# Kernel optimization log

Measured on AMD Instinct MI355X. Metric: run time of the kernel, lower is better.

Reference implementation:

```python
import jax, jax.numpy as jnp
import numpy as np

B, L, F, P = 128, 256, 4, 4   # dialogs, dialog length, future/past links
IN, H, C = 1024, 256, 7
N = B * L


def _build_edges():
    # same structure as build_intra_graph: self-loop + F future + P past per node
    i = np.arange(L)
    ss, tt = [], []
    for d in range(-P, F + 1):
        j = i + d
        m = (j >= 0) & (j < L)
        ss.append(i[m]); tt.append(j[m])
    s = np.concatenate(ss); t = np.concatenate(tt)
    offs = (np.arange(B) * L)[:, None]
    S = (s[None, :] + offs).ravel()
    T = (t[None, :] + offs).ravel()
    return np.stack([S, T]).astype(np.int32)


def setup_inputs() -> dict:
    key = jax.random.key(0)
    ks = jax.random.split(key, 16)
    ei = _build_edges()
    speakers = np.asarray(jax.random.randint(ks[0], (N,), 0, 2), dtype=np.int32)
    rel = (speakers[ei[0]] * speakers[ei[1]]).astype(np.int32)
    sd_in = 1.0 / np.sqrt(IN)
    sd_h = 1.0 / np.sqrt(H)
    return {
        "input": jax.random.normal(ks[1], (N, IN), jnp.float32),
        "dialog_lengths": jnp.full((B,), L, jnp.int32),
        "speakers": jnp.asarray(speakers),
        "labels": jax.random.randint(ks[2], (N,), 0, C, jnp.int32),
        "edge_index": jnp.asarray(ei),
        "rel_type": jnp.asarray(rel),
        # RGCNConv(IN, H, num_relations=2): per-relation weight, root weight, bias
        "W_rgcn": jax.random.normal(ks[3], (2, IN, H), jnp.float32) * sd_in,
        "W_root": jax.random.normal(ks[4], (IN, H), jnp.float32) * sd_in,
        "b_rgcn": jax.random.normal(ks[5], (H,), jnp.float32) * 0.01,
        # GraphConv(H, H): lin_rel (on aggregated neighbors, with bias), lin_root (no bias)
        "W_rel": jax.random.normal(ks[6], (H, H), jnp.float32) * sd_h,
        "b_rel": jax.random.normal(ks[7], (H,), jnp.float32) * 0.01,
        "W_grt": jax.random.normal(ks[8], (H, H), jnp.float32) * sd_h,
        # skip_con: Linear(IN, H)
        "W_skip": jax.random.normal(ks[9], (IN, H), jnp.float32) * sd_in,
        "b_skip": jax.random.normal(ks[10], (H,), jnp.float32) * 0.01,
        # classify: Linear(H, C)
        "W_cls": jax.random.normal(ks[11], (H, C), jnp.float32) * sd_h,
        "b_cls": jax.random.normal(ks[12], (C,), jnp.float32) * 0.01,
    }


def reference(input, dialog_lengths, speakers, labels, edge_index, rel_type,
              W_rgcn, W_root, b_rgcn, W_rel, b_rel, W_grt,
              W_skip, b_skip, W_cls, b_cls):
    n = input.shape[0]
    src, dst = edge_index[0], edge_index[1]
    seg = jax.ops.segment_sum

    # --- RGCNConv: out_i = x_i @ W_root + b + sum_r mean_{j in N_r(i)} x_j @ W_r
    t = jnp.einsum('ni,rio->rno', input, W_rgcn)      # [2, N, H]
    msg = t[rel_type, src]                            # [E, H] relation-specific messages
    h = input @ W_root + b_rgcn
    for r in range(2):
        m = (rel_type == r).astype(input.dtype)       # [E]
        s = seg(msg * m[:, None], dst, num_segments=n)
        cnt = seg(m, dst, num_segments=n)
        h = h + s / jnp.maximum(cnt, 1.0)[:, None]    # mean aggregation per relation

    # --- GraphConv (aggr='add'): out_i = W_rel @ sum_j h_j + b_rel + W_grt @ h_i
    neigh = seg(h[src], dst, num_segments=n)          # [N, H]
    h2 = neigh @ W_rel + b_rel + h @ W_grt

    # --- skip connection + classifier
    out = (h2 + input @ W_skip + b_skip) @ W_cls + b_cls  # [N, C]

    # --- cross entropy (mean)
    logp = jax.nn.log_softmax(out, axis=-1)
    loss = -jnp.mean(jnp.take_along_axis(logp, labels[:, None].astype(jnp.int32), axis=1))
    return out, loss
```

## Files before the change

### kernel.cpp

```cpp
#include <hip/hip_runtime.h>

#define NN 32768
#define INF 1024
#define HF 256

typedef __bf16 bf16x8 __attribute__((ext_vector_type(8)));
typedef float f32x4 __attribute__((ext_vector_type(4)));
typedef unsigned short u16x8 __attribute__((ext_vector_type(8)));

__device__ __forceinline__ float bf2f(unsigned short u) {
  union { unsigned int i; float f; } v; v.i = ((unsigned int)u) << 16; return v.f;
}
__device__ __forceinline__ unsigned short f2bf(float f) {
  union { float f; unsigned int i; } v; v.f = f;
  unsigned int x = v.i;
  return (unsigned short)((x + 0x7fffu + ((x >> 16) & 1u)) >> 16);
}

__device__ __forceinline__ void ld_lds16(const unsigned short* g, unsigned short* l) {
  __builtin_amdgcn_global_load_lds(
      (__attribute__((address_space(1))) const unsigned int*)g,
      (__attribute__((address_space(3))) unsigned int*)l, 16, 0, 0);
}
__device__ __forceinline__ void ld_lds16v(const void* g, void* l) {
  __builtin_amdgcn_global_load_lds(
      (__attribute__((address_space(1))) const unsigned int*)g,
      (__attribute__((address_space(3))) unsigned int*)l, 16, 0, 0);
}

__device__ __forceinline__ bf16x8 cvt8(f32x4 lo, f32x4 hi) {
  union { unsigned int u[4]; bf16x8 v; } r;
  asm("v_cvt_pk_bf16_f32 %0, %1, %2" : "=v"(r.u[0]) : "v"(lo[0]), "v"(lo[1]));
  asm("v_cvt_pk_bf16_f32 %0, %1, %2" : "=v"(r.u[1]) : "v"(lo[2]), "v"(lo[3]));
  asm("v_cvt_pk_bf16_f32 %0, %1, %2" : "=v"(r.u[2]) : "v"(hi[0]), "v"(hi[1]));
  asm("v_cvt_pk_bf16_f32 %0, %1, %2" : "=v"(r.u[3]) : "v"(hi[2]), "v"(hi[3]));
  return r.v;
}

__global__ __launch_bounds__(256)
void diagcn_prep(const float* __restrict__ Wrgcn, const float* __restrict__ Wroot,
                 const float* __restrict__ Wskip, const float* __restrict__ Wgrt,
                 const float* __restrict__ Wrel, unsigned short* __restrict__ WbigT,
                 unsigned short* __restrict__ WsmT, float* __restrict__ loss) {
  int tb = blockIdx.x;
  if (tb == 0 && threadIdx.x == 0) loss[0] = 0.f;
  __shared__ float tile[64 * 65];
  const float* src;
  int k0, ncol0;
  unsigned short* dst;
  int ldd, nrow0;
  if (tb < 256) {
    int tn = tb >> 4, tk = tb & 15;
    int mat = tn >> 2;
    src = (mat == 0) ? Wrgcn : (mat == 1) ? (Wrgcn + 262144) : (mat == 2) ? Wroot : Wskip;
    k0 = tk * 64; ncol0 = (tn & 3) * 64;
    dst = WbigT; ldd = 1024; nrow0 = tn * 64;
  } else {
    int t2 = tb - 256;
    int tn = t2 >> 3, tk = t2 & 7;
    src = (tk < 4) ? Wgrt : Wrel;
    k0 = (tk & 3) * 64; ncol0 = tn * 64;
    dst = WsmT; ldd = 512; nrow0 = tn * 64;
  }
  int kdst0 = (tb < 256) ? k0 : (((tb - 256) & 7) * 64);
  int c = threadIdx.x & 63, rb = threadIdx.x >> 6;
#pragma unroll
  for (int it = 0; it < 16; ++it) {
    int r = rb + it * 4;
    tile[r * 65 + c] = src[(size_t)(k0 + r) * 256 + ncol0 + c];
  }
  __syncthreads();
  int kk = threadIdx.x & 63;
#pragma unroll
  for (int it = 0; it < 16; ++it) {
    int nn = rb + it * 4;
    dst[(size_t)(nrow0 + nn) * ldd + kdst0 + kk] = f2bf(tile[kk * 65 + nn]);
  }
}

__global__ __launch_bounds__(512, 1)
void diagcn_gemm1(const float* __restrict__ X, const unsigned short* __restrict__ BT,
                  unsigned short* __restrict__ Y) {
  __shared__ unsigned short SH[73728];
  const int tid = threadIdx.x;
  const int w = tid >> 6, lane = tid & 63;
  const int quad = lane >> 4, l15 = lane & 15;
  const int wm = w >> 2, wn = w & 3;
  const int b = blockIdx.x;
  const int wg = ((b & 7) << 6) + (b >> 3);
  const int m0 = (wg >> 2) << 8;
  const int n0 = (wg & 3) << 8;
  const int bbase = wn * 64 + l15;
  const int sw8 = ((quad ^ ((l15 >> 1) & 3)) << 3);
  const int csrc8 = (((lane & 3) ^ ((lane >> 3) & 3)) << 3);
  const float* gAf = X + (size_t)(m0 + w * 32 + (lane >> 3)) * 1024
                       + (((lane & 7) ^ (lane >> 3)) << 2);
  const unsigned short* gB0 = BT + (size_t)(n0 + w * 32 + (lane >> 2)) * 1024 + csrc8;
  const int c1o = (((2 * quad) ^ (l15 & 7)) << 2);
  const int c2o = c1o ^ 4;

  f32x4 acc[8][4] = {};

#define G1_STAGE(t, buf)                                                       \
  {                                                                            \
    unsigned short* aB = SH + (buf) * 24576 + w * 2048;                        \
    const float* gs = gAf + (t) * 32;                                          \
    ld_lds16v(gs,             aB);                                             \
    ld_lds16v(gs +  8 * 1024, aB +  512);                                      \
    ld_lds16v(gs + 16 * 1024, aB + 1024);                                      \
    ld_lds16v(gs + 24 * 1024, aB + 1536);                                      \
    unsigned short* bB = SH + (buf) * 24576 + 16384 + w * 1024;                \
    const unsigned short* gb = gB0 + (t) * 32;                                 \
    ld_lds16(gb, bB);                                                          \
    ld_lds16(gb + 16 * 1024, bB + 512);                                        \
  }

#define G1_COMPUTE(buf)                                                       \
  {                                                                           \
    const float* Af = (const float*)(SH + (buf) * 24576);                     \
    const unsigned short* Bs = SH + (buf) * 24576 + 16384;                    \
    bf16x8 bv[4];                                                             \
    _Pragma("unroll")                                                         \
    for (int j = 0; j < 4; ++j)                                               \
      bv[j] = *(const bf16x8*)&Bs[(bbase + j * 16) * 32 + sw8];               \
    __builtin_amdgcn_s_setprio(1);                                            \
    _Pragma("unroll")                                                         \
    for (int i = 0; i < 8; ++i) {                                             \
      int ra = wm * 128 + i * 16 + l15;                                       \
      const float* rp = Af + ra * 32;                                         \
      f32x4 lo = *(const f32x4*)(rp + c1o);                                   \
      f32x4 hi = *(const f32x4*)(rp + c2o);                                   \
      bf16x8 av = cvt8(lo, hi);                                               \
      _Pragma("unroll")                                                       \
      for (int j = 0; j < 4; ++j)                                             \
        acc[i][j] = __builtin_amdgcn_mfma_f32_16x16x32_bf16(av, bv[j], acc[i][j], 0, 0, 0); \
    }                                                                         \
    __builtin_amdgcn_s_setprio(0);                                            \
  }

  G1_STAGE(0, 0);
  G1_STAGE(1, 1);
  asm volatile("s_waitcnt vmcnt(6)" ::: "memory");
  __builtin_amdgcn_s_barrier();

#pragma unroll 1
  for (int t = 0; t < 30; ++t) {
    G1_STAGE(t + 2, (t + 2) % 3);
    G1_COMPUTE(t % 3);
    asm volatile("s_waitcnt vmcnt(6)" ::: "memory");
    __builtin_amdgcn_s_barrier();
  }
  G1_COMPUTE(0);
  asm volatile("s_waitcnt vmcnt(0)" ::: "memory");
  __builtin_amdgcn_s_barrier();
  G1_COMPUTE(1);
#undef G1_STAGE
#undef G1_COMPUTE

#pragma unroll
  for (int i = 0; i < 8; ++i)
#pragma unroll
    for (int j = 0; j < 4; ++j) {
      const int row = m0 + wm * 128 + i * 16 + quad * 4;
      const int col = n0 + wn * 64 + j * 16 + l15;
#pragma unroll
      for (int r = 0; r < 4; ++r)
        Y[(size_t)(row + r) * 1024 + col] = f2bf(acc[i][j][r]);
    }
}

__global__ __launch_bounds__(256)
void diagcn_h(const unsigned short* __restrict__ Y, const int* __restrict__ spk,
              const float* __restrict__ brgcn, unsigned short* __restrict__ A2) {
  int b = blockIdx.x;
  int wv = threadIdx.x >> 6, lane = threadIdx.x & 63;
  int half = lane >> 5, li = lane & 31, c0 = li << 3;
  int node = ((b & 7) << 12) + ((b >> 3) << 3) + wv * 2 + half;
  int p = node & 255, dbase = node - p;
  int si = spk[node];
  float a0[8] = {}, a1[8] = {};
  float n0 = 0.f, n1 = 0.f;
#pragma unroll
  for (int d = -4; d <= 4; ++d) {
    int pj = p + d;
    float w = (pj >= 0 && pj < 256) ? 1.f : 0.f;
    int jc = pj < 0 ? 0 : (pj > 255 ? 255 : pj);
    int nj = dbase + jc;
    int rel = si & spk[nj];
    u16x8 v = *(const u16x8*)&Y[(size_t)nj * 1024 + (rel << 8) + c0];
    float w1 = rel ? w : 0.f, w0 = rel ? 0.f : w;
#pragma unroll
    for (int k = 0; k < 8; ++k) {
      float f = bf2f(v[k]);
      a0[k] += f * w0; a1[k] += f * w1;
    }
    n0 += w0; n1 += w1;
  }
  u16x8 vr = *(const u16x8*)&Y[(size_t)node * 1024 + 512 + c0];
  float i0 = 1.f / fmaxf(n0, 1.f), i1 = 1.f / fmaxf(n1, 1.f);
  u16x8 u;
#pragma unroll
  for (int k = 0; k < 8; ++k)
    u[k] = f2bf(bf2f(vr[k]) + brgcn[c0 + k] + a0[k] * i0 + a1[k] * i1);
  *(u16x8*)&A2[(size_t)node * 512 + c0] = u;
}

__global__ __launch_bounds__(256)
void diagcn_neigh(unsigned short* __restrict__ A2) {
  int b = blockIdx.x;
  int wv = threadIdx.x >> 6, lane = threadIdx.x & 63;
  int half = lane >> 5, li = lane & 31, c0 = li << 3;
  int node = ((b & 7) << 12) + ((b >> 3) << 3) + wv * 2 + half;
  int p = node & 255, dbase = node - p;
  float s[8] = {};
#pragma unroll
  for (int d = -4; d <= 4; ++d) {
    int pj = p + d;
    float w = (pj >= 0 && pj < 256) ? 1.f : 0.f;
    int jc = pj < 0 ? 0 : (pj > 255 ? 255 : pj);
    u16x8 v = *(const u16x8*)&A2[(size_t)(dbase + jc) * 512 + c0];
#pragma unroll
    for (int k = 0; k < 8; ++k) s[k] += bf2f(v[k]) * w;
  }
  u16x8 u;
#pragma unroll
  for (int k = 0; k < 8; ++k) u[k] = f2bf(s[k]);
  *(u16x8*)&A2[(size_t)node * 512 + 256 + c0] = u;
}

__global__ __launch_bounds__(256)
void diagcn_gemm2(const unsigned short* __restrict__ A, const unsigned short* __restrict__ BT,
                  const unsigned short* __restrict__ Y, const float* __restrict__ Wcls,
                  const float* __restrict__ bcls, const float* __restrict__ brel,
                  const float* __restrict__ bskip, const int* __restrict__ labels,
                  float* __restrict__ out, float* __restrict__ loss) {
  const int K = 512;
  __shared__ unsigned short SH[40960];
  const int tid = threadIdx.x;
  const int w = tid >> 6, lane = tid & 63;
  const int quad = lane >> 4, l15 = lane & 15;
  const int b = blockIdx.x;
  const int m0 = (((b & 7) << 6) + (b >> 3)) << 6;
  const int rowg = lane >> 3;
  const int kbsw = (lane & 7) ^ rowg;

  f32x4 acc[16] = {};
  const unsigned short* Abase = A + (size_t)m0 * K + kbsw * 8;
  const unsigned short* Bbase = BT + kbsw * 8;
  const unsigned short* Ybase = Y + (size_t)(m0 + (lane >> 5)) * 1024 + 768 + (lane & 31) * 8;

#define G2_STAGE(t, buf)                                                        \
  {                                                                             \
    unsigned short* As_ = SH + (buf) * 20480;                                   \
    unsigned short* Bs_ = As_ + 4096;                                           \
    int k0_ = (t) * 64;                                                         \
    _Pragma("unroll")                                                           \
    for (int i = 0; i < 2; ++i) {                                               \
      int grp = w * 2 + i;                                                      \
      ld_lds16(Abase + (size_t)(grp * 8 + rowg) * K + k0_, &As_[grp * 512]);    \
    }                                                                           \
    _Pragma("unroll")                                                           \
    for (int i = 0; i < 8; ++i) {                                               \
      int grp = w * 8 + i;                                                      \
      ld_lds16(Bbase + (size_t)(grp * 8 + rowg) * K + k0_, &Bs_[grp * 512]);    \
    }                                                                           \
  }
#define G2_COMPUTE(buf)                                                         \
  {                                                                             \
    const unsigned short* As_ = SH + (buf) * 20480;                             \
    const unsigned short* Bs_ = As_ + 4096;                                     \
    _Pragma("unroll")                                                           \
    for (int ks = 0; ks < 2; ++ks) {                                            \
      int kb = ks * 4 + quad;                                                   \
      int ra = w * 16 + l15;                                                    \
      bf16x8 av = *(const bf16x8*)&As_[ra * 64 + ((kb ^ (ra & 7)) << 3)];       \
      _Pragma("unroll")                                                         \
      for (int j = 0; j < 16; ++j) {                                            \
        int rb2 = j * 16 + l15;                                                 \
        bf16x8 bv = *(const bf16x8*)&Bs_[rb2 * 64 + ((kb ^ (rb2 & 7)) << 3)];   \
        acc[j] = __builtin_amdgcn_mfma_f32_16x16x32_bf16(av, bv, acc[j], 0, 0, 0); \
      }                                                                         \
    }                                                                           \
  }

  G2_STAGE(0, 0);
  G2_STAGE(1, 1);
  asm volatile("s_waitcnt vmcnt(10)" ::: "memory");
  __builtin_amdgcn_s_barrier();

#pragma unroll 1
  for (int t = 0; t < 6; ++t) {
    G2_COMPUTE(t & 1);
    asm volatile("s_waitcnt lgkmcnt(0)" ::: "memory");
    __builtin_amdgcn_s_barrier();
    G2_STAGE(t + 2, t & 1);
    asm volatile("s_waitcnt vmcnt(10)" ::: "memory");
    __builtin_amdgcn_s_barrier();
  }
  G2_COMPUTE(0);
  asm volatile("s_waitcnt lgkmcnt(0)" ::: "memory");
  __builtin_amdgcn_s_barrier();
  asm volatile("s_waitcnt vmcnt(0)" ::: "memory");
  __builtin_amdgcn_s_barrier();
#pragma unroll
  for (int i = 0; i < 8; ++i) {
    int g = w * 8 + i;
    ld_lds16(Ybase + (size_t)g * 2048, &SH[g * 512]);
  }
  G2_COMPUTE(1);
  asm volatile("s_waitcnt vmcnt(0)" ::: "memory");
  __builtin_amdgcn_s_barrier();

  float wsum[4][7] = {};
#pragma unroll
  for (int j = 0; j < 16; ++j) {
    int col = j * 16 + l15;
    float bb = brel[col] + bskip[col];
#pragma unroll
    for (int r = 0; r < 4; ++r) {
      int rl = w * 16 + quad * 4 + r;
      float z = acc[j][r] + bb + bf2f(SH[rl * 256 + col]);
#pragma unroll
      for (int c = 0; c < 7; ++c) wsum[r][c] += z * Wcls[col * 7 + c];
    }
  }
#pragma unroll
  for (int o = 1; o < 16; o <<= 1)
#pragma unroll
    for (int r = 0; r < 4; ++r)
#pragma unroll
      for (int c = 0; c < 7; ++c) wsum[r][c] += __shfl_xor(wsum[r][c], o, 64);

  float lsum = 0.f;
#pragma unroll
  for (int r = 0; r < 4; ++r) {
    int row = m0 + w * 16 + quad * 4 + r;
    float o7[7], mx = -1e30f;
#pragma unroll
    for (int c = 0; c < 7; ++c) {
      o7[c] = wsum[r][c] + bcls[c];
      mx = fmaxf(mx, o7[c]);
    }
    if (l15 < 7) out[(size_t)row * 7 + l15] = o7[l15];
    float s = 0.f;
#pragma unroll
    for (int c = 0; c < 7; ++c) s += expf(o7[c] - mx);
    int lab = labels[row];
    lsum += mx + logf(s) - o7[lab];
  }
  lsum += __shfl_xor(lsum, 16, 64);
  lsum += __shfl_xor(lsum, 32, 64);
  if (lane == 0) atomicAdd(loss, lsum * (1.0f / (float)NN));
#undef G2_STAGE
#undef G2_COMPUTE
}

extern "C" void kernel_launch(void* const* d_in, const int* in_sizes, int n_in,
                              void* d_out, int out_size, void* d_ws, size_t ws_size,
                              hipStream_t stream) {
  const float* x      = (const float*)d_in[0];
  const int* speakers = (const int*)d_in[2];
  const int* labels   = (const int*)d_in[3];
  const float* Wrgcn  = (const float*)d_in[6];
  const float* Wroot  = (const float*)d_in[7];
  const float* brgcn  = (const float*)d_in[8];
  const float* Wrel   = (const float*)d_in[9];
  const float* brel   = (const float*)d_in[10];
  const float* Wgrt   = (const float*)d_in[11];
  const float* Wskip  = (const float*)d_in[12];
  const float* bskip  = (const float*)d_in[13];
  const float* Wcls   = (const float*)d_in[14];
  const float* bcls   = (const float*)d_in[15];
  float* out = (float*)d_out;
  float* loss = out + (size_t)NN * 7;

  const size_t OFF_WBIG = 0;
  const size_t OFF_WSM  = 2097152;
  const size_t OFF_Y    = 2359296;
  const size_t OFF_A2   = 69468160;
  const size_t NEED     = 103022592;
  if (ws_size < NEED) return;

  char* ws = (char*)d_ws;
  unsigned short* WbigT = (unsigned short*)(ws + OFF_WBIG);
  unsigned short* WsmT  = (unsigned short*)(ws + OFF_WSM);
  unsigned short* Y     = (unsigned short*)(ws + OFF_Y);
  unsigned short* A2    = (unsigned short*)(ws + OFF_A2);

  diagcn_prep<<<dim3(288), dim3(256), 0, stream>>>(Wrgcn, Wroot, Wskip, Wgrt, Wrel,
                                                   WbigT, WsmT, loss);
  diagcn_gemm1<<<dim3(512), dim3(512), 0, stream>>>(x, WbigT, Y);
  diagcn_h<<<dim3(NN / 8), dim3(256), 0, stream>>>(Y, speakers, brgcn, A2);
  diagcn_neigh<<<dim3(NN / 8), dim3(256), 0, stream>>>(A2);
  diagcn_gemm2<<<dim3(512), dim3(256), 0, stream>>>(A2, WsmT, Y, Wcls, bcls, brel, bskip,
                                                    labels, out, loss);
}
```

Measured before the change: 361.9 us.

## Shrink gemm1 tile to 128x256, convert A to bf16 before LDS

The first GEMM now uses 128-row tiles over 1024 blocks instead of 256-row tiles over 512. The fp32 A operand is loaded into registers and converted to bf16 once before being written to shared memory, rather than staged as fp32 via global_load_lds and converted inside the MFMA loop. This halves the LDS footprint and launch bounds allow several blocks per CU, aiming at more occupancy and less per-MFMA conversion work. The trade-off is that B tiles are re-read from global memory twice as often, and the A path now goes through registers with explicit waits.

```diff
diff --git a/kernel.cpp b/kernel.cpp
--- a/kernel.cpp
+++ b/kernel.cpp
@@ -22,14 +22,9 @@
       (__attribute__((address_space(1))) const unsigned int*)g,
       (__attribute__((address_space(3))) unsigned int*)l, 16, 0, 0);
 }
-__device__ __forceinline__ void ld_lds16v(const void* g, void* l) {
-  __builtin_amdgcn_global_load_lds(
-      (__attribute__((address_space(1))) const unsigned int*)g,
-      (__attribute__((address_space(3))) unsigned int*)l, 16, 0, 0);
-}
-
-__device__ __forceinline__ bf16x8 cvt8(f32x4 lo, f32x4 hi) {
-  union { unsigned int u[4]; bf16x8 v; } r;
+
+__device__ __forceinline__ u16x8 cvt8u(f32x4 lo, f32x4 hi) {
+  union { unsigned int u[4]; u16x8 v; } r;
   asm("v_cvt_pk_bf16_f32 %0, %1, %2" : "=v"(r.u[0]) : "v"(lo[0]), "v"(lo[1]));
   asm("v_cvt_pk_bf16_f32 %0, %1, %2" : "=v"(r.u[1]) : "v"(lo[2]), "v"(lo[3]));
   asm("v_cvt_pk_bf16_f32 %0, %1, %2" : "=v"(r.u[2]) : "v"(hi[0]), "v"(hi[1]));
@@ -78,90 +73,96 @@
   }
 }
 
-__global__ __launch_bounds__(512, 1)
+__global__ __launch_bounds__(512, 4)
 void diagcn_gemm1(const float* __restrict__ X, const unsigned short* __restrict__ BT,
                   unsigned short* __restrict__ Y) {
-  __shared__ unsigned short SH[73728];
+  __shared__ unsigned short SH[36864];
   const int tid = threadIdx.x;
   const int w = tid >> 6, lane = tid & 63;
   const int quad = lane >> 4, l15 = lane & 15;
   const int wm = w >> 2, wn = w & 3;
   const int b = blockIdx.x;
-  const int wg = ((b & 7) << 6) + (b >> 3);
-  const int m0 = (wg >> 2) << 8;
+  const int wg = ((b & 7) << 7) + (b >> 3);
+  const int m0 = (wg >> 2) << 7;
   const int n0 = (wg & 3) << 8;
-  const int bbase = wn * 64 + l15;
   const int sw8 = ((quad ^ ((l15 >> 1) & 3)) << 3);
   const int csrc8 = (((lane & 3) ^ ((lane >> 3) & 3)) << 3);
-  const float* gAf = X + (size_t)(m0 + w * 32 + (lane >> 3)) * 1024
-                       + (((lane & 7) ^ (lane >> 3)) << 2);
+  const float* gAx = X + (size_t)(m0 + (tid >> 2)) * 1024 + ((tid & 3) << 3);
   const unsigned short* gB0 = BT + (size_t)(n0 + w * 32 + (lane >> 2)) * 1024 + csrc8;
-  const int c1o = (((2 * quad) ^ (l15 & 7)) << 2);
-  const int c2o = c1o ^ 4;
-
-  f32x4 acc[8][4] = {};
-
-#define G1_STAGE(t, buf)                                                       \
-  {                                                                            \
-    unsigned short* aB = SH + (buf) * 24576 + w * 2048;                        \
-    const float* gs = gAf + (t) * 32;                                          \
-    ld_lds16v(gs,             aB);                                             \
-    ld_lds16v(gs +  8 * 1024, aB +  512);                                      \
-    ld_lds16v(gs + 16 * 1024, aB + 1024);                                      \
-    ld_lds16v(gs + 24 * 1024, aB + 1536);                                      \
-    unsigned short* bB = SH + (buf) * 24576 + 16384 + w * 1024;                \
-    const unsigned short* gb = gB0 + (t) * 32;                                 \
-    ld_lds16(gb, bB);                                                          \
-    ld_lds16(gb + 16 * 1024, bB + 512);                                        \
-  }
-
-#define G1_COMPUTE(buf)                                                       \
-  {                                                                           \
-    const float* Af = (const float*)(SH + (buf) * 24576);                     \
-    const unsigned short* Bs = SH + (buf) * 24576 + 16384;                    \
-    bf16x8 bv[4];                                                             \
-    _Pragma("unroll")                                                         \
-    for (int j = 0; j < 4; ++j)                                               \
-      bv[j] = *(const bf16x8*)&Bs[(bbase + j * 16) * 32 + sw8];               \
-    __builtin_amdgcn_s_setprio(1);                                            \
-    _Pragma("unroll")                                                         \
-    for (int i = 0; i < 8; ++i) {                                             \
-      int ra = wm * 128 + i * 16 + l15;                                       \
-      const float* rp = Af + ra * 32;                                         \
-      f32x4 lo = *(const f32x4*)(rp + c1o);                                   \
-      f32x4 hi = *(const f32x4*)(rp + c2o);                                   \
-      bf16x8 av = cvt8(lo, hi);                                               \
-      _Pragma("unroll")                                                       \
-      for (int j = 0; j < 4; ++j)                                             \
+  const int dA = (tid >> 2) * 32 + ((tid & 3) << 3);
+
+  f32x4 acc[4][4] = {};
+  f32x4 s0, s1;
+
+#define G1_COMPUTE(buf)                                                           \
+  {                                                                               \
+    const unsigned short* Ab = &SH[(buf) * 12288];                                \
+    const unsigned short* Bb = &SH[(buf) * 12288 + 4096];                         \
+    bf16x8 bv[4];                                                                 \
+    _Pragma("unroll")                                                             \
+    for (int j = 0; j < 4; ++j)                                                   \
+      bv[j] = *(const bf16x8*)&Bb[(wn * 64 + j * 16 + l15) * 32 + sw8];           \
+    __builtin_amdgcn_s_setprio(1);                                                \
+    _Pragma("unroll")                                                             \
+    for (int i = 0; i < 4; ++i) {                                                 \
+      bf16x8 av = *(const bf16x8*)&Ab[(wm * 64 + i * 16 + l15) * 32 + quad * 8];  \
+      _Pragma("unroll")                                                           \
+      for (int j = 0; j < 4; ++j)                                                 \
         acc[i][j] = __builtin_amdgcn_mfma_f32_16x16x32_bf16(av, bv[j], acc[i][j], 0, 0, 0); \
-    }                                                                         \
-    __builtin_amdgcn_s_setprio(0);                                            \
-  }
-
-  G1_STAGE(0, 0);
-  G1_STAGE(1, 1);
-  asm volatile("s_waitcnt vmcnt(6)" ::: "memory");
+    }                                                                             \
+    __builtin_amdgcn_s_setprio(0);                                                \
+  }
+
+  s0 = *(const f32x4*)(gAx);
+  s1 = *(const f32x4*)(gAx + 4);
+  {
+    unsigned short* bB = &SH[4096 + w * 1024];
+    ld_lds16(gB0, bB);
+    ld_lds16(gB0 + 16 * 1024, bB + 512);
+  }
+  *(u16x8*)&SH[dA] = cvt8u(s0, s1);
+  s0 = *(const f32x4*)(gAx + 32);
+  s1 = *(const f32x4*)(gAx + 36);
+  {
+    unsigned short* bB = &SH[12288 + 4096 + w * 1024];
+    ld_lds16(gB0 + 32, bB);
+    ld_lds16(gB0 + 32 + 16 * 1024, bB + 512);
+  }
+  asm volatile("s_waitcnt vmcnt(4)" ::: "memory");
+  asm volatile("s_waitcnt lgkmcnt(0)");
+  __builtin_amdgcn_sched_barrier(0);
   __builtin_amdgcn_s_barrier();
 
 #pragma unroll 1
   for (int t = 0; t < 30; ++t) {
-    G1_STAGE(t + 2, (t + 2) % 3);
+    *(u16x8*)&SH[((t + 1) % 3) * 12288 + dA] = cvt8u(s0, s1);
+    s0 = *(const f32x4*)(gAx + (t + 2) * 32);
+    s1 = *(const f32x4*)(gAx + (t + 2) * 32 + 4);
+    {
+      unsigned short* bB = &SH[((t + 2) % 3) * 12288 + 4096 + w * 1024];
+      ld_lds16(gB0 + (t + 2) * 32, bB);
+      ld_lds16(gB0 + (t + 2) * 32 + 16 * 1024, bB + 512);
+    }
     G1_COMPUTE(t % 3);
-    asm volatile("s_waitcnt vmcnt(6)" ::: "memory");
+    asm volatile("s_waitcnt vmcnt(4)" ::: "memory");
+    asm volatile("s_waitcnt lgkmcnt(0)");
+    __builtin_amdgcn_sched_barrier(0);
     __builtin_amdgcn_s_barrier();
   }
-  G1_COMPUTE(0);
+  *(u16x8*)&SH[(31 % 3) * 12288 + dA] = cvt8u(s0, s1);
+  G1_COMPUTE(30 % 3);
   asm volatile("s_waitcnt vmcnt(0)" ::: "memory");
-  __builtin_amdgcn_s_barrier();
-  G1_COMPUTE(1);
-#undef G1_STAGE
+  asm volatile("s_waitcnt lgkmcnt(0)");
+  __builtin_amdgcn_sched_barrier(0);
+  __builtin_amdgcn_s_barrier();
+  G1_COMPUTE(31 % 3);
 #undef G1_COMPUTE
 
 #pragma unroll
-  for (int i = 0; i < 8; ++i)
+  for (int i = 0; i < 4; ++i)
 #pragma unroll
     for (int j = 0; j < 4; ++j) {
-      const int row = m0 + wm * 128 + i * 16 + quad * 4;
+      const int row = m0 + wm * 64 + i * 16 + quad * 4;
       const int col = n0 + wn * 64 + j * 16 + l15;
 #pragma unroll
       for (int r = 0; r < 4; ++r)
@@ -389,7 +390,7 @@
 
   diagcn_prep<<<dim3(288), dim3(256), 0, stream>>>(Wrgcn, Wroot, Wskip, Wgrt, Wrel,
                                                    WbigT, WsmT, loss);
-  diagcn_gemm1<<<dim3(512), dim3(512), 0, stream>>>(x, WbigT, Y);
+  diagcn_gemm1<<<dim3(1024), dim3(512), 0, stream>>>(x, WbigT, Y);
   diagcn_h<<<dim3(NN / 8), dim3(256), 0, stream>>>(Y, speakers, brgcn, A2);
   diagcn_neigh<<<dim3(NN / 8), dim3(256), 0, stream>>>(A2);
   diagcn_gemm2<<<dim3(512), dim3(256), 0, stream>>>(A2, WsmT, Y, Wcls, bcls, brel, bskip,
```

Result: slower. 386.5 us (+6.8%).
